# Kernel tuning notes

Measured on AMD Instinct MI355X. Metric: run time of the kernel, lower is better.

The kernel has to match this reference:

```python
import jax, jax.numpy as jnp
import numpy as np

N_NODES = 50000
N_EDGES = 600000
D = 128
THETA = (0.5, -1.0, 0.5)  # len(theta) must be 3 to match learnable_diag[3, in_feats]


def setup_inputs() -> dict:
    key = jax.random.key(0)
    k1, k2, k3, k4, k5 = jax.random.split(key, 5)
    feat = jax.random.normal(k1, (N_NODES, D), dtype=jnp.float32)
    edge_index = jax.random.randint(k2, (2, N_EDGES), 0, N_NODES)  # [src; dst]
    # learnable_diag = torch.rand(3, in_feats)
    diag = jax.random.uniform(k3, (3, D), dtype=jnp.float32)
    # nn.Linear(out_feats, out_feats) with xavier_uniform weight, zero bias
    limit = float(np.sqrt(6.0 / (D + D)))
    W = jax.random.uniform(k4, (D, D), dtype=jnp.float32, minval=-limit, maxval=limit)
    b = jnp.zeros((D,), dtype=jnp.float32)
    return {"feat": feat, "edge_index": edge_index, "diag": diag, "W": W, "b": b}


def reference(feat, edge_index, diag, W, b):
    src, dst = edge_index[0], edge_index[1]
    n = feat.shape[0]
    # in_degrees: count of incoming edges per node
    deg = jax.ops.segment_sum(jnp.ones_like(dst, dtype=feat.dtype), dst, num_segments=n)
    d_invsqrt = jnp.clip(deg, 1.0, None) ** -0.5  # [N]
    d_invsqrt = d_invsqrt[:, None]  # [N,1]

    h = (THETA[0] * feat) * diag[0]
    h = h @ W.T + b  # nn.Linear

    for k in range(1, len(THETA)):
        # unnLaplacian: feat - (A @ (feat * Dinv)) * Dinv * diag[k]
        msg = feat * d_invsqrt  # [N,D]
        agg = jax.ops.segment_sum(msg[src], dst, num_segments=n)  # SpMM: copy_u + sum
        feat = feat - agg * d_invsqrt * diag[k]
        h = h + THETA[k] * feat
    return h
```

## Files before the change

### kernel.cpp

```cpp
#include <hip/hip_runtime.h>

#define NN 50000
#define NE 600000
#define D  128
#define NBLK 196

typedef __attribute__((ext_vector_type(8))) short bf16x8;
typedef __attribute__((ext_vector_type(4))) float floatx4;
typedef __attribute__((ext_vector_type(2))) float f32x2;

__device__ __forceinline__ unsigned short bf16_rne(float f) {
    union { float f; unsigned u; } v; v.f = f;
    unsigned r = v.u + 0x7FFFu + ((v.u >> 16) & 1u);
    return (unsigned short)(r >> 16);
}
__device__ __forceinline__ unsigned pack2(float a, float b) {
    return (unsigned)bf16_rne(a) | ((unsigned)bf16_rne(b) << 16);
}

__global__ __launch_bounds__(256) void prep_kernel(const float* __restrict__ W,
                                                   const float* __restrict__ diag,
                                                   unsigned short* __restrict__ Wb,
                                                   int* __restrict__ deg_i,
                                                   unsigned int* __restrict__ zrow0,
                                                   unsigned int* __restrict__ zrow1) {
    int g = blockIdx.x * 256 + threadIdx.x;
    if (g < NN) deg_i[g] = 0;
    if (g < 16384) {
        int j = g & 127;
        Wb[g] = bf16_rne(0.5f * diag[j] * W[g]);
    }
    if (g < 64) { zrow0[g] = 0u; zrow1[g] = 0u; }
}

__global__ __launch_bounds__(256) void hist_kernel(const int* __restrict__ dst,
                                                   int* __restrict__ deg_i) {
    int e = blockIdx.x * 256 + threadIdx.x;
    if (e < NE) atomicAdd(&deg_i[dst[e]], 1);
}

__global__ __launch_bounds__(256) void scan1_kernel(const int* __restrict__ deg_i,
                                                    int* __restrict__ row_ptr,
                                                    int* __restrict__ partials,
                                                    float* __restrict__ dinvf,
                                                    float* __restrict__ rdegf) {
    __shared__ int sh[256];
    int i = blockIdx.x * 256 + threadIdx.x;
    int dg = (i < NN) ? deg_i[i] : 0;
    if (i < NN) {
        float d = (float)dg;
        float dc = d > 1.0f ? d : 1.0f;
        dinvf[i] = rsqrtf(dc);
        rdegf[i] = sqrtf(dc);
    }
    sh[threadIdx.x] = dg;
    __syncthreads();
    #pragma unroll
    for (int off = 1; off < 256; off <<= 1) {
        int t = (threadIdx.x >= off) ? sh[threadIdx.x - off] : 0;
        __syncthreads();
        sh[threadIdx.x] += t;
        __syncthreads();
    }
    if (i < NN) row_ptr[i + 1] = sh[threadIdx.x];
    if (threadIdx.x == 255) partials[blockIdx.x] = sh[255];
}

__global__ __launch_bounds__(256) void scan23_kernel(int* __restrict__ row_ptr,
                                                     const int* __restrict__ partials) {
    __shared__ int sh[256];
    const int t = threadIdx.x;
    sh[t] = (t < NBLK) ? partials[t] : 0;
    __syncthreads();
    #pragma unroll
    for (int off = 1; off < 256; off <<= 1) {
        int v = (t >= off) ? sh[t - off] : 0;
        __syncthreads();
        sh[t] += v;
        __syncthreads();
    }
    const int add = (blockIdx.x > 0) ? sh[blockIdx.x - 1] : 0;
    const int i = blockIdx.x * 256 + t;
    if (i < NN) row_ptr[i + 1] += add;
    if (i == 0) row_ptr[0] = 0;
}

__global__ __launch_bounds__(256) void fill_kernel(const int* __restrict__ src,
                                                   const int* __restrict__ dst,
                                                   const int* __restrict__ row_ptr,
                                                   int* __restrict__ deg_i,
                                                   int* __restrict__ csr) {
    int e = blockIdx.x * 256 + threadIdx.x;
    if (e < NE) {
        int t = dst[e];
        int c = atomicAdd(&deg_i[t], -1);
        csr[row_ptr[t] + c - 1] = src[e];
    }
}

__global__ __launch_bounds__(256) void gemm_mfma_kernel(const float* __restrict__ feat,
                                                        const unsigned short* __restrict__ Wb,
                                                        const float* __restrict__ b,
                                                        const float* __restrict__ dinvf,
                                                        unsigned short* __restrict__ featb_s,
                                                        float* __restrict__ out) {
    const int wv   = threadIdx.x >> 6;
    const int lane = threadIdx.x & 63;
    const int r16  = lane & 15;
    const int quad = lane >> 4;
    const int m0   = blockIdx.x * 64 + wv * 16;

    const int mrow = m0 + r16;
    const int mc   = (mrow < NN) ? mrow : (NN - 1);
    const float* arow = feat + (size_t)mc * D + quad * 8;
    const float di = dinvf[mc];

    bf16x8 afrag[4];
    #pragma unroll
    for (int kc = 0; kc < 4; ++kc) {
        const float4 f0 = *(const float4*)(arow + kc * 32);
        const float4 f1 = *(const float4*)(arow + kc * 32 + 4);
        bf16x8 a;
        a[0] = (short)bf16_rne(f0.x); a[1] = (short)bf16_rne(f0.y);
        a[2] = (short)bf16_rne(f0.z); a[3] = (short)bf16_rne(f0.w);
        a[4] = (short)bf16_rne(f1.x); a[5] = (short)bf16_rne(f1.y);
        a[6] = (short)bf16_rne(f1.z); a[7] = (short)bf16_rne(f1.w);
        afrag[kc] = a;
        if (mrow < NN) {
            uint4 st;
            st.x = pack2(f0.x * di, f0.y * di);
            st.y = pack2(f0.z * di, f0.w * di);
            st.z = pack2(f1.x * di, f1.y * di);
            st.w = pack2(f1.z * di, f1.w * di);
            *(uint4*)(featb_s + (size_t)mc * D + quad * 8 + kc * 32) = st;
        }
    }

    floatx4 acc[8];
    #pragma unroll
    for (int nt = 0; nt < 8; ++nt) acc[nt] = (floatx4)(0.0f);

    #pragma unroll
    for (int nt = 0; nt < 8; ++nt) {
        const unsigned short* brow = Wb + (size_t)(nt * 16 + r16) * D + quad * 8;
        #pragma unroll
        for (int kc = 0; kc < 4; ++kc) {
            const bf16x8 bfrag = *(const bf16x8*)(brow + kc * 32);
            acc[nt] = __builtin_amdgcn_mfma_f32_16x16x32_bf16(afrag[kc], bfrag, acc[nt], 0, 0, 0);
        }
    }

    #pragma unroll
    for (int nt = 0; nt < 8; ++nt) {
        const int d = nt * 16 + r16;
        const float bd = b[d];
        #pragma unroll
        for (int r = 0; r < 4; ++r) {
            const int i = m0 + quad * 4 + r;
            if (i < NN) out[(size_t)i * D + d] = acc[nt][r] + bd;
        }
    }
}

__device__ __forceinline__ floatx4 gather_acc(const unsigned short* __restrict__ rows,
                                              const int* __restrict__ csr,
                                              int e0, int e1, int lane) {
    const int half = lane >> 5;
    const unsigned lane_b = (unsigned)((lane & 31) << 3);
    f32x2 a01 = (f32x2)(0.0f);
    f32x2 a23 = (f32x2)(0.0f);
    for (int bse = e0; bse < e1; bse += 64) {
        int idx = bse + lane;
        int s = (idx < e1) ? csr[idx] : NN;
        int cnt8 = (min(64, e1 - bse) + 7) & ~7;
        for (int k = 0; k < cnt8; k += 8) {
            #pragma unroll
            for (int u = 0; u < 4; ++u) {
                int ss = __shfl(s, k + 2 * u + half);
                const uint2 pv = *(const uint2*)((const char*)rows +
                                    (((unsigned)ss << 8) | lane_b));
                f32x2 lo0, lo1;
                lo0.x = __uint_as_float(pv.x << 16);
                lo0.y = __uint_as_float(pv.x & 0xFFFF0000u);
                lo1.x = __uint_as_float(pv.y << 16);
                lo1.y = __uint_as_float(pv.y & 0xFFFF0000u);
                a01 += lo0;
                a23 += lo1;
            }
        }
    }
    floatx4 r;
    r[0] = a01.x; r[1] = a01.y; r[2] = a23.x; r[3] = a23.y;
    #pragma unroll
    for (int i = 0; i < 4; ++i) r[i] += __shfl_xor(r[i], 32);
    return r;
}

__global__ __launch_bounds__(256) void gather1_kernel(const unsigned short* __restrict__ featb_s,
                                                      const int* __restrict__ csr,
                                                      const int* __restrict__ row_ptr,
                                                      const float* __restrict__ dinvf,
                                                      const float* __restrict__ diag,
                                                      const float* __restrict__ feat0,
                                                      unsigned short* __restrict__ feat1s) {
    const int node = blockIdx.x * 4 + (threadIdx.x >> 6);
    const int lane = threadIdx.x & 63;
    floatx4 acc = gather_acc(featb_s, csr, row_ptr[node], row_ptr[node + 1], lane);
    if (lane < 32) {
        const int c0 = lane << 2;
        const float di = dinvf[node];
        const float4 bs = *(const float4*)(feat0 + (size_t)node * D + c0);
        const float4 dg = *(const float4*)(diag + D + c0);
        const float r0 = (bs.x - acc[0] * di * dg.x) * di;
        const float r1 = (bs.y - acc[1] * di * dg.y) * di;
        const float r2 = (bs.z - acc[2] * di * dg.z) * di;
        const float r3 = (bs.w - acc[3] * di * dg.w) * di;
        uint2 st; st.x = pack2(r0, r1); st.y = pack2(r2, r3);
        *(uint2*)((char*)feat1s + ((size_t)node << 8) + (lane << 3)) = st;
    }
}

__global__ __launch_bounds__(256) void gather2_kernel(const unsigned short* __restrict__ feat1s,
                                                      const int* __restrict__ csr,
                                                      const int* __restrict__ row_ptr,
                                                      const float* __restrict__ dinvf,
                                                      const float* __restrict__ rdegf,
                                                      const float* __restrict__ diag,
                                                      float* __restrict__ outp) {
    const int node = blockIdx.x * 4 + (threadIdx.x >> 6);
    const int lane = threadIdx.x & 63;
    floatx4 acc = gather_acc(feat1s, csr, row_ptr[node], row_ptr[node + 1], lane);
    if (lane < 32) {
        const int c0 = lane << 2;
        const float di = dinvf[node];
        const float rd = rdegf[node];
        const uint2 bp = *(const uint2*)((const char*)feat1s + ((size_t)node << 8) + (lane << 3));
        const float b0 = __uint_as_float(bp.x << 16) * rd;
        const float b1 = __uint_as_float(bp.x & 0xFFFF0000u) * rd;
        const float b2 = __uint_as_float(bp.y << 16) * rd;
        const float b3 = __uint_as_float(bp.y & 0xFFFF0000u) * rd;
        const float4 dg = *(const float4*)(diag + 2 * D + c0);
        float4 cur = *(float4*)(outp + (size_t)node * D + c0);
        cur.x -= 0.5f * (b0 + acc[0] * di * dg.x);
        cur.y -= 0.5f * (b1 + acc[1] * di * dg.y);
        cur.z -= 0.5f * (b2 + acc[2] * di * dg.z);
        cur.w -= 0.5f * (b3 + acc[3] * di * dg.w);
        *(float4*)(outp + (size_t)node * D + c0) = cur;
    }
}

extern "C" void kernel_launch(void* const* d_in, const int* in_sizes, int n_in,
                              void* d_out, int out_size, void* d_ws, size_t ws_size,
                              hipStream_t stream) {
    const float* feat = (const float*)d_in[0];
    const int*   eidx = (const int*)d_in[1];
    const float* diag = (const float*)d_in[2];
    const float* W    = (const float*)d_in[3];
    const float* b    = (const float*)d_in[4];
    float* out = (float*)d_out;

    const int* src = eidx;
    const int* dst = eidx + NE;

    unsigned short* featb_s = (unsigned short*)d_ws;
    unsigned short* feat1s  = featb_s + (size_t)(NN + 1) * D;
    int*   csr      = (int*)(feat1s + (size_t)(NN + 1) * D);
    float* dinvf    = (float*)(csr + NE);
    float* rdegf    = dinvf + NN;
    int*   deg_i    = (int*)(rdegf + NN);
    int*   row_ptr  = deg_i + NN;
    int*   partials = row_ptr + NN + 2;
    unsigned short* Wb = (unsigned short*)(partials + 256);

    prep_kernel<<<NBLK, 256, 0, stream>>>(W, diag, Wb, deg_i,
                                          (unsigned int*)(featb_s + (size_t)NN * D),
                                          (unsigned int*)(feat1s + (size_t)NN * D));

    hist_kernel<<<(NE + 255) / 256, 256, 0, stream>>>(dst, deg_i);
    scan1_kernel<<<NBLK, 256, 0, stream>>>(deg_i, row_ptr, partials, dinvf, rdegf);
    scan23_kernel<<<NBLK, 256, 0, stream>>>(row_ptr, partials);
    fill_kernel<<<(NE + 255) / 256, 256, 0, stream>>>(src, dst, row_ptr, deg_i, csr);

    gemm_mfma_kernel<<<(NN + 63) / 64, 256, 0, stream>>>(feat, Wb, b, dinvf, featb_s, out);

    gather1_kernel<<<NN / 4, 256, 0, stream>>>(featb_s, csr, row_ptr, dinvf, diag,
                                               feat, feat1s);
    gather2_kernel<<<NN / 4, 256, 0, stream>>>(feat1s, csr, row_ptr, dinvf, rdegf, diag, out);
}
```

Baseline: 222.4 us.

## Fuse CSR build kernels into one cooperative kernel with grid syncs

Merges the five setup kernels (prep, histogram, two scan stages, fill) into one cooperative-launched kernel with a grid-stride loop and grid.sync barriers between phases. The aim is to remove the launch overhead and inter-kernel gaps of the five small kernels. In exchange, each grid.sync costs a device-wide barrier, and a grid of 1024 blocks must be co-resident for the cooperative launch to succeed.

```diff
diff --git a/kernel.cpp b/kernel.cpp
--- a/kernel.cpp
+++ b/kernel.cpp
@@ -1,9 +1,13 @@
 #include <hip/hip_runtime.h>
+#include <hip/hip_cooperative_groups.h>
+
+namespace cg = cooperative_groups;
 
 #define NN 50000
 #define NE 600000
 #define D  128
 #define NBLK 196
+#define SETUP_GRID 1024
 
 typedef __attribute__((ext_vector_type(8))) short bf16x8;
 typedef __attribute__((ext_vector_type(4))) float floatx4;
@@ -18,83 +22,80 @@
     return (unsigned)bf16_rne(a) | ((unsigned)bf16_rne(b) << 16);
 }
 
-__global__ __launch_bounds__(256) void prep_kernel(const float* __restrict__ W,
-                                                   const float* __restrict__ diag,
-                                                   unsigned short* __restrict__ Wb,
-                                                   int* __restrict__ deg_i,
-                                                   unsigned int* __restrict__ zrow0,
-                                                   unsigned int* __restrict__ zrow1) {
-    int g = blockIdx.x * 256 + threadIdx.x;
-    if (g < NN) deg_i[g] = 0;
-    if (g < 16384) {
-        int j = g & 127;
-        Wb[g] = bf16_rne(0.5f * diag[j] * W[g]);
-    }
-    if (g < 64) { zrow0[g] = 0u; zrow1[g] = 0u; }
-}
-
-__global__ __launch_bounds__(256) void hist_kernel(const int* __restrict__ dst,
-                                                   int* __restrict__ deg_i) {
-    int e = blockIdx.x * 256 + threadIdx.x;
-    if (e < NE) atomicAdd(&deg_i[dst[e]], 1);
-}
-
-__global__ __launch_bounds__(256) void scan1_kernel(const int* __restrict__ deg_i,
+__global__ __launch_bounds__(256) void setup_kernel(const int* __restrict__ src,
+                                                    const int* __restrict__ dst,
+                                                    const float* __restrict__ W,
+                                                    const float* __restrict__ diag,
+                                                    unsigned short* __restrict__ Wb,
+                                                    int* __restrict__ deg_i,
                                                     int* __restrict__ row_ptr,
                                                     int* __restrict__ partials,
                                                     float* __restrict__ dinvf,
-                                                    float* __restrict__ rdegf) {
-    __shared__ int sh[256];
-    int i = blockIdx.x * 256 + threadIdx.x;
-    int dg = (i < NN) ? deg_i[i] : 0;
-    if (i < NN) {
-        float d = (float)dg;
-        float dc = d > 1.0f ? d : 1.0f;
-        dinvf[i] = rsqrtf(dc);
-        rdegf[i] = sqrtf(dc);
-    }
-    sh[threadIdx.x] = dg;
-    __syncthreads();
-    #pragma unroll
-    for (int off = 1; off < 256; off <<= 1) {
-        int t = (threadIdx.x >= off) ? sh[threadIdx.x - off] : 0;
-        __syncthreads();
-        sh[threadIdx.x] += t;
-        __syncthreads();
-    }
-    if (i < NN) row_ptr[i + 1] = sh[threadIdx.x];
-    if (threadIdx.x == 255) partials[blockIdx.x] = sh[255];
-}
-
-__global__ __launch_bounds__(256) void scan23_kernel(int* __restrict__ row_ptr,
-                                                     const int* __restrict__ partials) {
+                                                    float* __restrict__ rdegf,
+                                                    int* __restrict__ csr,
+                                                    unsigned int* __restrict__ zrow0,
+                                                    unsigned int* __restrict__ zrow1) {
+    cg::grid_group grid = cg::this_grid();
     __shared__ int sh[256];
     const int t = threadIdx.x;
-    sh[t] = (t < NBLK) ? partials[t] : 0;
-    __syncthreads();
-    #pragma unroll
-    for (int off = 1; off < 256; off <<= 1) {
-        int v = (t >= off) ? sh[t - off] : 0;
+    const int gid = blockIdx.x * 256 + t;
+    const int gstride = SETUP_GRID * 256;
+
+    for (int i = gid; i < NN; i += gstride) deg_i[i] = 0;
+    if (gid < 16384) {
+        int j = gid & 127;
+        Wb[gid] = bf16_rne(0.5f * diag[j] * W[gid]);
+    }
+    if (gid < 64) { zrow0[gid] = 0u; zrow1[gid] = 0u; }
+    grid.sync();
+
+    for (int e = gid; e < NE; e += gstride) atomicAdd(&deg_i[dst[e]], 1);
+    grid.sync();
+
+    if (blockIdx.x < NBLK) {
+        const int i = blockIdx.x * 256 + t;
+        int dg = (i < NN) ? deg_i[i] : 0;
+        if (i < NN) {
+            float d = (float)dg;
+            float dc = d > 1.0f ? d : 1.0f;
+            dinvf[i] = rsqrtf(dc);
+            rdegf[i] = sqrtf(dc);
+        }
+        sh[t] = dg;
         __syncthreads();
-        sh[t] += v;
+        #pragma unroll
+        for (int off = 1; off < 256; off <<= 1) {
+            int v = (t >= off) ? sh[t - off] : 0;
+            __syncthreads();
+            sh[t] += v;
+            __syncthreads();
+        }
+        if (i < NN) row_ptr[i + 1] = sh[t];
+        if (t == 255) partials[blockIdx.x] = sh[255];
+    }
+    grid.sync();
+
+    if (blockIdx.x < NBLK) {
+        sh[t] = (t < NBLK) ? partials[t] : 0;
         __syncthreads();
-    }
-    const int add = (blockIdx.x > 0) ? sh[blockIdx.x - 1] : 0;
-    const int i = blockIdx.x * 256 + t;
-    if (i < NN) row_ptr[i + 1] += add;
-    if (i == 0) row_ptr[0] = 0;
-}
-
-__global__ __launch_bounds__(256) void fill_kernel(const int* __restrict__ src,
-                                                   const int* __restrict__ dst,
-                                                   const int* __restrict__ row_ptr,
-                                                   int* __restrict__ deg_i,
-                                                   int* __restrict__ csr) {
-    int e = blockIdx.x * 256 + threadIdx.x;
-    if (e < NE) {
-        int t = dst[e];
-        int c = atomicAdd(&deg_i[t], -1);
-        csr[row_ptr[t] + c - 1] = src[e];
+        #pragma unroll
+        for (int off = 1; off < 256; off <<= 1) {
+            int v = (t >= off) ? sh[t - off] : 0;
+            __syncthreads();
+            sh[t] += v;
+            __syncthreads();
+        }
+        const int add = (blockIdx.x > 0) ? sh[blockIdx.x - 1] : 0;
+        const int i = blockIdx.x * 256 + t;
+        if (i < NN) row_ptr[i + 1] += add;
+        if (i == 0) row_ptr[0] = 0;
+    }
+    grid.sync();
+
+    for (int e = gid; e < NE; e += gstride) {
+        int tt = dst[e];
+        int c = atomicAdd(&deg_i[tt], -1);
+        csr[row_ptr[tt] + c - 1] = src[e];
     }
 }
 
@@ -272,14 +273,15 @@
     int*   partials = row_ptr + NN + 2;
     unsigned short* Wb = (unsigned short*)(partials + 256);
 
-    prep_kernel<<<NBLK, 256, 0, stream>>>(W, diag, Wb, deg_i,
-                                          (unsigned int*)(featb_s + (size_t)NN * D),
-                                          (unsigned int*)(feat1s + (size_t)NN * D));
-
-    hist_kernel<<<(NE + 255) / 256, 256, 0, stream>>>(dst, deg_i);
-    scan1_kernel<<<NBLK, 256, 0, stream>>>(deg_i, row_ptr, partials, dinvf, rdegf);
-    scan23_kernel<<<NBLK, 256, 0, stream>>>(row_ptr, partials);
-    fill_kernel<<<(NE + 255) / 256, 256, 0, stream>>>(src, dst, row_ptr, deg_i, csr);
+    unsigned int* zr0 = (unsigned int*)(featb_s + (size_t)NN * D);
+    unsigned int* zr1 = (unsigned int*)(feat1s + (size_t)NN * D);
+
+    void* args[] = { (void*)&src, (void*)&dst, (void*)&W, (void*)&diag, (void*)&Wb,
+                     (void*)&deg_i, (void*)&row_ptr, (void*)&partials,
+                     (void*)&dinvf, (void*)&rdegf, (void*)&csr,
+                     (void*)&zr0, (void*)&zr1 };
+    hipLaunchCooperativeKernel((const void*)setup_kernel, dim3(SETUP_GRID), dim3(256),
+                               args, 0, stream);
 
     gemm_mfma_kernel<<<(NN + 63) / 64, 256, 0, stream>>>(feat, Wb, b, dinvf, featb_s, out);
 
```

Measured after the change: 605.9 us. +172.4%, slower.
